# Performance work log

Measured on AMD Instinct MI355X. Metric: run time of the kernel, lower is better.

The kernel has to match this reference:

```python
import jax, jax.numpy as jnp
import numpy as np

BETA = 0.25  # commitment cost


def setup_inputs() -> dict:
    key = jax.random.key(0)
    k1, k2 = jax.random.split(key)
    B, C, T = 16, 256, 1024      # batch, emb_dim channels, sequence length
    N_EMB = 8192                 # codebook size
    z = jax.random.normal(k1, (B, C, T), dtype=jnp.float32)
    # original init: uniform(-1/n_emb, 1/n_emb); scale a normal similarly small
    emb = jax.random.normal(k2, (N_EMB, C), dtype=jnp.float32) * (1.0 / N_EMB)
    return {"z": z, "emb": emb}


def reference(z, emb):
    sg = jax.lax.stop_gradient
    # [B, C, T] -> [B, T, C]
    zt = jnp.transpose(z, (0, 2, 1))
    B, T, C = zt.shape
    zf = zt.reshape(-1, C)  # [B*T, C]
    # squared euclidean distances: ||z||^2 + ||e||^2 - 2 z.e  -> [B*T, N]
    d = (jnp.sum(zf * zf, axis=1, keepdims=True)
         + jnp.sum(emb * emb, axis=1)
         - 2.0 * jnp.einsum('bd,nd->bn', zf, emb))
    idx = jnp.argmin(d, axis=-1)               # [B*T]
    z_q = emb[idx].reshape(B, T, C)            # [B, T, C]
    loss = (BETA * jnp.mean((sg(z_q) - zt) ** 2)
            + jnp.mean((z_q - sg(zt)) ** 2))
    # straight-through estimator
    z_q = zt + sg(z_q - zt)
    z_q = jnp.transpose(z_q, (0, 2, 1))        # back to [B, C, T]
    return z_q, loss, idx
```

## Files before the change

### kernel.cpp

```cpp
#include <hip/hip_runtime.h>


#define C_    256
#define T_    1024
#define M_    16384
#define N_    8192

#define OUT_ZQ   0
#define OUT_LOSS 4194304
#define OUT_IDX  4194305

#define WS_SZ    0
#define WS_SE    16384
#define WS_PART  24576
#define MIN_OFF  131072u
#define FB_OFF   8519680u
#define WS_NEED  16908288u
#define O_I1     24576
#define O_I2     40960
#define O_PART   73728

typedef __attribute__((ext_vector_type(8))) short bf16x8;
typedef __attribute__((ext_vector_type(4))) float f32x4;
typedef unsigned long long ull;

__device__ __forceinline__ unsigned short f2b(float f) {
    unsigned u = __float_as_uint(f);
    return (unsigned short)((u + 0x7FFFu + ((u >> 16) & 1u)) >> 16);
}
__device__ __forceinline__ float b2f(unsigned short u) {
    return __uint_as_float(((unsigned)u) << 16);
}

__global__ __launch_bounds__(256) void vq_sums(const float* __restrict__ z,
                                               const float* __restrict__ emb,
                                               float* __restrict__ ws) {
    int gid = blockIdx.x * 256 + threadIdx.x;
    if (gid < M_) {
        int b = gid >> 10, t = gid & (T_ - 1);
        const float* zp = z + (size_t)b * C_ * T_ + t;
        float blk[2];
#pragma unroll
        for (int h = 0; h < 2; ++h) {
            float r[8];
#pragma unroll
            for (int j = 0; j < 8; ++j) {
                float v = zp[(size_t)(h * 128 + j) * T_];
                r[j] = __fmul_rn(v, v);
            }
            for (int i = 8; i < 128; i += 8)
#pragma unroll
                for (int j = 0; j < 8; ++j) {
                    float v = zp[(size_t)(h * 128 + i + j) * T_];
                    r[j] = __fadd_rn(r[j], __fmul_rn(v, v));
                }
            blk[h] = __fadd_rn(__fadd_rn(__fadd_rn(r[0], r[1]), __fadd_rn(r[2], r[3])),
                               __fadd_rn(__fadd_rn(r[4], r[5]), __fadd_rn(r[6], r[7])));
        }
        ws[WS_SZ + gid] = __fadd_rn(blk[0], blk[1]);
    } else if (gid < M_ + N_) {
        int n = gid - M_;
        const float* ep = emb + (size_t)n * C_;
        float blk[2];
#pragma unroll
        for (int h = 0; h < 2; ++h) {
            float r[8];
#pragma unroll
            for (int j = 0; j < 8; ++j) {
                float v = ep[h * 128 + j];
                r[j] = __fmul_rn(v, v);
            }
            for (int i = 8; i < 128; i += 8)
#pragma unroll
                for (int j = 0; j < 8; ++j) {
                    float v = ep[h * 128 + i + j];
                    r[j] = __fadd_rn(r[j], __fmul_rn(v, v));
                }
            blk[h] = __fadd_rn(__fadd_rn(__fadd_rn(r[0], r[1]), __fadd_rn(r[2], r[3])),
                               __fadd_rn(__fadd_rn(r[4], r[5]), __fadd_rn(r[6], r[7])));
        }
        ws[WS_SE + n] = __fadd_rn(blk[0], blk[1]);
    }
}

__global__ __launch_bounds__(256) void vq_prep_b(const float* __restrict__ emb,
                                                 char* __restrict__ fb) {
    int gid = blockIdx.x * 256 + threadIdx.x;
    int n = gid >> 5, kg = gid & 31;
    const float* ep = emb + (size_t)n * C_ + kg * 8;
    unsigned hi[8], lo[8];
#pragma unroll
    for (int j = 0; j < 8; ++j) {
        float v = ep[j];
        unsigned short h = f2b(v);
        hi[j] = h;
        lo[j] = f2b(v - b2f(h));
    }
    int nt = n >> 4, kt = kg >> 2, lane = (kg & 3) * 16 + (n & 15);
    size_t base = ((size_t)((nt * 8 + kt) * 2) << 10) + (lane << 4);
    uint4 hv = {hi[0] | (hi[1] << 16), hi[2] | (hi[3] << 16), hi[4] | (hi[5] << 16), hi[6] | (hi[7] << 16)};
    uint4 lv = {lo[0] | (lo[1] << 16), lo[2] | (lo[3] << 16), lo[4] | (lo[5] << 16), lo[6] | (lo[7] << 16)};
    *(uint4*)(fb + base) = hv;
    *(uint4*)(fb + base + 1024) = lv;
}

__global__ __launch_bounds__(256, 2) void vq_mfma2(
        const float* __restrict__ z, const char* __restrict__ fb,
        const float* __restrict__ sz, const float* __restrict__ se,
        ull* __restrict__ minima) {
    __shared__ __align__(16) char ldsA[65536];
    __shared__ __align__(16) char ldsB[16384];

    const int tid = threadIdx.x;
    const int lane = tid & 63;
    const int w = tid >> 6, wm = w & 1, wn = w >> 1;
    const int quad = lane >> 4, li = lane & 15;
    const int mb = blockIdx.x, ns = blockIdx.y;

    {
        const float* zb = z + (size_t)(mb >> 4) * C_ * T_ + ((mb & 15) << 6);
#pragma unroll
        for (int p = 0; p < 4; ++p) {
            int c  = p * 64 + (tid >> 2);
            int tq = tid & 3;
            const float* src = zb + (size_t)c * T_ + tq * 16;
            int kt = c >> 5, kg3 = (c >> 3) & 3, j = c & 7;
            unsigned short* d0 = (unsigned short*)(ldsA + (((tq * 8 + kt) * 2 + 0) << 10) + (kg3 << 8) + (j << 1));
            unsigned short* d1 = (unsigned short*)(ldsA + (((tq * 8 + kt) * 2 + 1) << 10) + (kg3 << 8) + (j << 1));
#pragma unroll
            for (int u = 0; u < 4; ++u) {
                float4 v = *(const float4*)(src + u * 4);
                float vv[4] = {v.x, v.y, v.z, v.w};
#pragma unroll
                for (int e = 0; e < 4; ++e) {
                    unsigned short h = f2b(vv[e]);
                    unsigned short l = f2b(vv[e] - b2f(h));
                    int i = u * 4 + e;
                    d0[i * 8] = h;
                    d1[i * 8] = l;
                }
            }
        }
    }

    float szr[8];
#pragma unroll
    for (int mt = 0; mt < 2; ++mt)
#pragma unroll
        for (int r = 0; r < 4; ++r)
            szr[mt * 4 + r] = sz[(mb << 6) + (wm << 5) + (mt << 4) + (quad << 2) + r];

    ull key[8];
#pragma unroll
    for (int s = 0; s < 8; ++s) key[s] = ~0ULL;

    const int f = tid >> 4, pos = (tid & 15) << 4;

    for (int nt = 0; nt < 32; ++nt) {
        f32x4 acc[2][4];
#pragma unroll
        for (int i = 0; i < 2; ++i)
#pragma unroll
            for (int j = 0; j < 4; ++j) acc[i][j] = (f32x4){0.f, 0.f, 0.f, 0.f};
        const int ntile0 = ns * 256 + nt * 8;

        for (int kt = 0; kt < 8; ++kt) {
            __syncthreads();
            {
                const char* srcB = fb + ((((size_t)(ntile0 + (f >> 1)) * 8 + kt) * 2 + (f & 1)) << 10) + pos;
                char* dB = ldsB + (f << 10) + pos;
#pragma unroll
                for (int i = 0; i < 4; ++i)
                    *(uint4*)(dB + i * 256) = *(const uint4*)(srcB + i * 256);
            }
            __syncthreads();
            bf16x8 a[2][2];
#pragma unroll
            for (int mt = 0; mt < 2; ++mt) {
                a[mt][0] = *(const bf16x8*)(ldsA + ((((wm * 2 + mt) * 8 + kt) * 2 + 0) << 10) + (lane << 4));
                a[mt][1] = *(const bf16x8*)(ldsA + ((((wm * 2 + mt) * 8 + kt) * 2 + 1) << 10) + (lane << 4));
            }
#pragma unroll
            for (int nt4 = 0; nt4 < 4; ++nt4) {
                bf16x8 bh = *(const bf16x8*)(ldsB + ((((wn * 4 + nt4) * 2 + 0)) << 10) + (lane << 4));
                bf16x8 bl = *(const bf16x8*)(ldsB + ((((wn * 4 + nt4) * 2 + 1)) << 10) + (lane << 4));
#pragma unroll
                for (int mt = 0; mt < 2; ++mt) {
                    f32x4 c = acc[mt][nt4];
                    c = __builtin_amdgcn_mfma_f32_16x16x32_bf16(a[mt][0], bh, c, 0, 0, 0);
                    c = __builtin_amdgcn_mfma_f32_16x16x32_bf16(a[mt][0], bl, c, 0, 0, 0);
                    c = __builtin_amdgcn_mfma_f32_16x16x32_bf16(a[mt][1], bh, c, 0, 0, 0);
                    acc[mt][nt4] = c;
                }
            }
        }
#pragma unroll
        for (int nt4 = 0; nt4 < 4; ++nt4) {
            const int ncol = ns * 4096 + nt * 128 + (wn * 4 + nt4) * 16 + li;
            const float sev = se[ncol];
#pragma unroll
            for (int mt = 0; mt < 2; ++mt) {
                f32x4 c = acc[mt][nt4];
#pragma unroll
                for (int r = 0; r < 4; ++r) {
                    float s = fmaf(-2.f, c[r], __fadd_rn(szr[mt * 4 + r], sev));
                    ull k = ((ull)__float_as_uint(s) << 32) | (unsigned)ncol;
                    int sl = mt * 4 + r;
                    if (k < key[sl]) key[sl] = k;
                }
            }
        }
        if (nt & 1) {
            int sc = nt >> 1;
#pragma unroll
            for (int sl = 0; sl < 8; ++sl) {
                ull kk = key[sl];
#pragma unroll
                for (int off = 1; off <= 8; off <<= 1) {
                    ull o = __shfl_xor(kk, off, 64);
                    if (o < kk) kk = o;
                }
                if (li == 0) {
                    int row = (mb << 6) + (wm << 5) + ((sl >> 2) << 4) + (quad << 2) + (sl & 3);
                    minima[(size_t)row * 64 + ((ns * 16 + sc) * 2 + wn)] = kk;
                }
                key[sl] = ~0ULL;
            }
        }
    }
}

__global__ __launch_bounds__(256) void vq_pick2(
        const float* __restrict__ z, const float* __restrict__ emb,
        const float* __restrict__ ws, const ull* __restrict__ minima,
        float* __restrict__ out) {
    __shared__ float Lz[256 * 17];
    const float* sz = ws + WS_SZ;
    const float* se = ws + WS_SE;
    const int tid = threadIdx.x;
    const int w = tid >> 6, lane = tid & 63, li = lane & 15;
    const int m0 = blockIdx.x * 16;
    const int b = m0 >> 10, t0 = m0 & (T_ - 1);

    {
        const float* src = z + (size_t)b * C_ * T_ + (size_t)tid * T_ + t0;
#pragma unroll
        for (int u = 0; u < 4; ++u) {
            float4 v = *(const float4*)(src + u * 4);
            Lz[tid * 17 + u * 4 + 0] = v.x;
            Lz[tid * 17 + u * 4 + 1] = v.y;
            Lz[tid * 17 + u * 4 + 2] = v.z;
            Lz[tid * 17 + u * 4 + 3] = v.w;
        }
    }
    __syncthreads();

    for (int rr = 0; rr < 4; ++rr) {
        const int tloc = w * 4 + rr;
        const int m = m0 + tloc;
        ull kmin = minima[(size_t)m * 64 + lane];
        int cand[4];
#pragma unroll
        for (int rep = 0; rep < 4; ++rep) {
            ull bf = kmin;
#pragma unroll
            for (int off = 1; off <= 32; off <<= 1) {
                ull o = __shfl_xor(bf, off, 64);
                if (o < bf) bf = o;
            }
            int ix = (int)(unsigned)(bf & 0xFFFFFFFFull);
            cand[rep] = ix < 0 ? 0 : (ix > N_ - 1 ? N_ - 1 : ix);
            if (kmin == bf) kmin = ~0ULL;
        }
        const int cn = cand[lane >> 4];
        const float* ep = emb + (size_t)cn * C_;
        double sum = 0.0;
#pragma unroll
        for (int cc = 0; cc < 16; ++cc) {
            int c = cc * 16 + li;
            sum = fma((double)Lz[c * 17 + tloc], (double)ep[c], sum);
        }
#pragma unroll
        for (int off = 1; off <= 8; off <<= 1)
            sum += __shfl_xor(sum, off, 64);
        double s0 = __shfl(sum, 0, 64), s1 = __shfl(sum, 16, 64);
        double s2 = __shfl(sum, 32, 64), s3 = __shfl(sum, 48, 64);
        if (lane == 0) {
            float szm = sz[m];
            float d0 = fmaf(-2.f, (float)s0, __fadd_rn(szm, se[cand[0]]));
            float d1 = fmaf(-2.f, (float)s1, __fadd_rn(szm, se[cand[1]]));
            float d2 = fmaf(-2.f, (float)s2, __fadd_rn(szm, se[cand[2]]));
            float d3 = fmaf(-2.f, (float)s3, __fadd_rn(szm, se[cand[3]]));
            float bd = d0; int bi = cand[0];
            if (d1 < bd || (d1 == bd && cand[1] < bi)) { bd = d1; bi = cand[1]; }
            if (d2 < bd || (d2 == bd && cand[2] < bi)) { bd = d2; bi = cand[2]; }
            if (d3 < bd || (d3 == bd && cand[3] < bi)) { bd = d3; bi = cand[3]; }
            out[OUT_IDX + m] = (float)bi;
        }
    }
}

__global__ __launch_bounds__(256) void vq_pass1_fp32(
        const float* __restrict__ z,
        const float* __restrict__ emb,
        float* __restrict__ ws) {
    __shared__ float As[32][68];
    __shared__ float Bs[32][68];
    const float* s_z = ws + WS_SZ;
    const float* s_e = ws + WS_SE;
    int* i1ws = (int*)ws + O_I1;
    int* i2ws = (int*)ws + O_I2;
    const int tid = threadIdx.x;
    const int mt  = blockIdx.x;
    const int tx  = tid & 15, ty = tid >> 4;
    const int b   = mt >> 4;
    const int t0  = (mt << 6) & (T_ - 1);
    const float* zbase = z + (size_t)b * C_ * T_ + t0;
    const int a_k = tid >> 4;
    const int a_m = (tid & 15) << 2;
    const int b_j = tid >> 2;
    const int b_q = (tid & 3) << 3;
    const float4 sz4 = *(const float4*)(s_z + mt * 64 + (ty << 2));
    const float szv[4] = {sz4.x, sz4.y, sz4.z, sz4.w};
    float v1[4], v2[4];
    int   i1[4], i2[4];
#pragma unroll
    for (int i = 0; i < 4; ++i) {
        v1[i] = INFINITY; v2[i] = INFINITY;
        i1[i] = 0x7FFFFFFF; i2[i] = 0x7FFFFFFF;
    }
    for (int nt = 0; nt < N_ / 64; ++nt) {
        const int n0 = nt * 64;
        float acc[4][4];
#pragma unroll
        for (int i = 0; i < 4; ++i)
#pragma unroll
            for (int j = 0; j < 4; ++j) acc[i][j] = 0.f;
        for (int kt = 0; kt < C_; kt += 32) {
            __syncthreads();
#pragma unroll
            for (int p = 0; p < 2; ++p) {
                int k = a_k + p * 16;
                float4 af = *(const float4*)(zbase + (size_t)(kt + k) * T_ + a_m);
                *(float4*)&As[k][a_m] = af;
            }
            {
                const float* ep = emb + (size_t)(n0 + b_j) * C_ + kt + b_q;
                float4 e0 = ((const float4*)ep)[0];
                float4 e1 = ((const float4*)ep)[1];
                Bs[b_q + 0][b_j] = e0.x; Bs[b_q + 1][b_j] = e0.y;
                Bs[b_q + 2][b_j] = e0.z; Bs[b_q + 3][b_j] = e0.w;
                Bs[b_q + 4][b_j] = e1.x; Bs[b_q + 5][b_j] = e1.y;
                Bs[b_q + 6][b_j] = e1.z; Bs[b_q + 7][b_j] = e1.w;
            }
            __syncthreads();
#pragma unroll
            for (int k = 0; k < 32; ++k) {
                const float4 a  = *(const float4*)&As[k][ty << 2];
                const float4 bv = *(const float4*)&Bs[k][tx << 2];
                acc[0][0] = fmaf(a.x, bv.x, acc[0][0]);
                acc[0][1] = fmaf(a.x, bv.y, acc[0][1]);
                acc[0][2] = fmaf(a.x, bv.z, acc[0][2]);
                acc[0][3] = fmaf(a.x, bv.w, acc[0][3]);
                acc[1][0] = fmaf(a.y, bv.x, acc[1][0]);
                acc[1][1] = fmaf(a.y, bv.y, acc[1][1]);
                acc[1][2] = fmaf(a.y, bv.z, acc[1][2]);
                acc[1][3] = fmaf(a.y, bv.w, acc[1][3]);
                acc[2][0] = fmaf(a.z, bv.x, acc[2][0]);
                acc[2][1] = fmaf(a.z, bv.y, acc[2][1]);
                acc[2][2] = fmaf(a.z, bv.z, acc[2][2]);
                acc[2][3] = fmaf(a.z, bv.w, acc[2][3]);
                acc[3][0] = fmaf(a.w, bv.x, acc[3][0]);
                acc[3][1] = fmaf(a.w, bv.y, acc[3][1]);
                acc[3][2] = fmaf(a.w, bv.z, acc[3][2]);
                acc[3][3] = fmaf(a.w, bv.w, acc[3][3]);
            }
        }
        const float4 se4 = *(const float4*)(s_e + n0 + (tx << 2));
        const float sev[4] = {se4.x, se4.y, se4.z, se4.w};
#pragma unroll
        for (int j = 0; j < 4; ++j) {
            const int n = n0 + (tx << 2) + j;
#pragma unroll
            for (int i = 0; i < 4; ++i) {
                float A = __fadd_rn(szv[i], sev[j]);
                float s = fmaf(-2.f, acc[i][j], A);
                if (s < v1[i]) { v2[i] = v1[i]; i2[i] = i1[i]; v1[i] = s; i1[i] = n; }
                else if (s < v2[i]) { v2[i] = s; i2[i] = n; }
            }
        }
    }
#pragma unroll
    for (int i = 0; i < 4; ++i) {
        float a1 = v1[i], a2 = v2[i];
        int   y1 = i1[i], y2 = i2[i];
#pragma unroll
        for (int off = 8; off >= 1; off >>= 1) {
            float o1 = __shfl_xor(a1, off, 64); int p1 = __shfl_xor(y1, off, 64);
            float o2 = __shfl_xor(a2, off, 64); int p2 = __shfl_xor(y2, off, 64);
            bool alt = (o1 < a1) || (o1 == a1 && p1 < y1);
            float w1 = alt ? o1 : a1; int q1 = alt ? p1 : y1;
            float lv = alt ? a1 : o1; int lq = alt ? y1 : p1;
            float wv = alt ? o2 : a2; int wq = alt ? p2 : y2;
            bool sb = (lv < wv) || (lv == wv && lq < wq);
            a2 = sb ? lv : wv; y2 = sb ? lq : wq;
            a1 = w1; y1 = q1;
        }
        if (tx == 0) {
            int m = mt * 64 + (ty << 2) + i;
            i1ws[m] = y1;
            i2ws[m] = y2;
        }
    }
}

__global__ __launch_bounds__(256) void vq_pass2_fp32(
        const float* __restrict__ z,
        const float* __restrict__ emb,
        float* __restrict__ ws,
        float* __restrict__ out) {
    const float* s_z = ws + WS_SZ;
    const float* s_e = ws + WS_SE;
    const int* i1ws = (const int*)ws + O_I1;
    const int* i2ws = (const int*)ws + O_I2;
    const int tid  = threadIdx.x;
    const int wave = tid >> 6, lane = tid & 63;
    const int half = lane >> 5;
    const int c0   = (lane & 31) << 3;
    const int rowbase = (blockIdx.x * 4 + wave) * 64;
    for (int r = 0; r < 64; ++r) {
        const int m = rowbase + r;
        int c1 = i1ws[m], c2 = i2ws[m];
        c1 = c1 < 0 ? 0 : (c1 > N_ - 1 ? N_ - 1 : c1);
        c2 = c2 < 0 ? 0 : (c2 > N_ - 1 ? N_ - 1 : c2);
        const int b = m >> 10, t = m & (T_ - 1);
        const float* zp = z + (size_t)b * C_ * T_ + t;
        const int cand = half ? c2 : c1;
        const float* ep = emb + (size_t)cand * C_;
        double sum = 0.0;
#pragma unroll
        for (int c = 0; c < 8; ++c)
            sum = fma((double)zp[(size_t)(c0 + c) * T_], (double)ep[c0 + c], sum);
#pragma unroll
        for (int off = 1; off <= 16; off <<= 1)
            sum += __shfl_xor(sum, off, 64);
        double s1 = __shfl(sum, 0, 64);
        double s2 = __shfl(sum, 32, 64);
        if (lane == 0) {
            float p1 = (float)s1, p2 = (float)s2;
            float d1 = fmaf(-2.f, p1, __fadd_rn(s_z[m], s_e[c1]));
            float d2 = fmaf(-2.f, p2, __fadd_rn(s_z[m], s_e[c2]));
            int win = ((d2 < d1) || (d2 == d1 && c2 < c1)) ? c2 : c1;
            out[OUT_IDX + m] = (float)win;
        }
    }
}

__global__ __launch_bounds__(256) void vq_gather(
        const float* __restrict__ z,
        const float* __restrict__ emb,
        float* __restrict__ partial,
        float* __restrict__ out) {
    __shared__ float Ls[64][129];
    __shared__ int   idxs[64];
    __shared__ float wred[4];
    const int tid = threadIdx.x;
    const int mg  = blockIdx.x;
    const int m0  = mg << 6;
    const int b   = m0 >> 10;
    const int t0  = m0 & (T_ - 1);
    if (tid < 64) {
        int ix = (int)out[OUT_IDX + m0 + tid];
        idxs[tid] = ix < 0 ? 0 : (ix > N_ - 1 ? N_ - 1 : ix);
    }
    __syncthreads();
    float lsum = 0.f;
    const int w = tid >> 6, l = tid & 63;
    const int tt2 = tid & 63, c0 = tid >> 6;
    const size_t base = (size_t)b * (C_ * T_) + t0 + tt2;
#pragma unroll
    for (int ch = 0; ch < 2; ++ch) {
        __syncthreads();
#pragma unroll
        for (int it = 0; it < 8; ++it) {
            int tt = it * 8 + w * 2 + (l >> 5);
            int cq = l & 31;
            int row = idxs[tt];
            float4 ev = *(const float4*)(emb + (size_t)row * C_ + ch * 128 + (cq << 2));
            Ls[tt][(cq << 2) + 0] = ev.x;
            Ls[tt][(cq << 2) + 1] = ev.y;
            Ls[tt][(cq << 2) + 2] = ev.z;
            Ls[tt][(cq << 2) + 3] = ev.w;
        }
        __syncthreads();
#pragma unroll
        for (int st = 0; st < 32; ++st) {
            int c_l = (st << 2) + c0;
            int c   = (ch << 7) + c_l;
            float v = Ls[tt2][c_l];
            size_t off = base + (size_t)c * T_;
            out[OUT_ZQ + off] = v;
            float d = v - z[off];
            lsum = fmaf(d, d, lsum);
        }
    }
#pragma unroll
    for (int off = 32; off >= 1; off >>= 1) lsum += __shfl_xor(lsum, off, 64);
    if (l == 0) wred[w] = lsum;
    __syncthreads();
    if (tid == 0) partial[mg] = wred[0] + wred[1] + wred[2] + wred[3];
}

__global__ __launch_bounds__(256) void vq_loss(const float* __restrict__ partial,
                                               float* __restrict__ out) {
    __shared__ float wred[4];
    const int tid = threadIdx.x;
    float v = partial[tid];
#pragma unroll
    for (int off = 32; off >= 1; off >>= 1) v += __shfl_xor(v, off, 64);
    if ((tid & 63) == 0) wred[tid >> 6] = v;
    __syncthreads();
    if (tid == 0)
        out[OUT_LOSS] = (wred[0] + wred[1] + wred[2] + wred[3]) * (1.25f / 4194304.f);
}

extern "C" void kernel_launch(void* const* d_in, const int* in_sizes, int n_in,
                              void* d_out, int out_size, void* d_ws, size_t ws_size,
                              hipStream_t stream) {
    const float* z   = (const float*)d_in[0];
    const float* emb = (const float*)d_in[1];
    float* out = (float*)d_out;
    float* ws  = (float*)d_ws;

    vq_sums<<<dim3((M_ + N_) / 256), dim3(256), 0, stream>>>(z, emb, ws);

    if (ws_size >= WS_NEED) {
        char* fb = (char*)d_ws + FB_OFF;
        ull* minima = (ull*)((char*)d_ws + MIN_OFF);
        vq_prep_b<<<dim3(1024), dim3(256), 0, stream>>>(emb, fb);
        vq_mfma2<<<dim3(256, 2), dim3(256), 0, stream>>>(z, fb, ws + WS_SZ, ws + WS_SE, minima);
        vq_pick2<<<dim3(1024), dim3(256), 0, stream>>>(z, emb, ws, minima, out);
        vq_gather<<<dim3(M_ / 64), dim3(256), 0, stream>>>(z, emb, ws + WS_PART, out);
        vq_loss<<<dim3(1), dim3(256), 0, stream>>>(ws + WS_PART, out);
    } else {
        vq_pass1_fp32<<<dim3(M_ / 64), dim3(256), 0, stream>>>(z, emb, ws);
        vq_pass2_fp32<<<dim3(64), dim3(256), 0, stream>>>(z, emb, ws, out);
        vq_gather<<<dim3(M_ / 64), dim3(256), 0, stream>>>(z, emb, ws + O_PART, out);
        vq_loss<<<dim3(1), dim3(256), 0, stream>>>(ws + O_PART, out);
    }
}
```

Measured before the change: 371.5 us.

## Stream codebook tiles straight into registers and drop LDS B staging

The distance GEMM kernel no longer stages codebook tiles through shared memory with two barriers per k-step. Each wave now loads its own B fragments directly from global memory into registers, double-buffered across k-steps, and computes all four M-subtiles against four N-subtiles. Block indices are remapped so the two codebook halves for neighbouring z blocks run close together, and minima are kept at a finer granularity (128 partial keys per row), which the pick kernel merges pairwise. This removes LDS traffic and barrier stalls, but raises register pressure, increases global/L2 loads of B, and enlarges the minima workspace.

After: 514.8 us. 1.39x slower.

```diff
diff --git a/kernel.cpp b/kernel.cpp
--- a/kernel.cpp
+++ b/kernel.cpp
@@ -14,8 +14,8 @@
 #define WS_SE    16384
 #define WS_PART  24576
 #define MIN_OFF  131072u
-#define FB_OFF   8519680u
-#define WS_NEED  16908288u
+#define FB_OFF   16908288u
+#define WS_NEED  25296896u
 #define O_I1     24576
 #define O_I2     40960
 #define O_PART   73728
@@ -104,18 +104,20 @@
     *(uint4*)(fb + base + 1024) = lv;
 }
 
-__global__ __launch_bounds__(256, 2) void vq_mfma2(
+__global__ __launch_bounds__(256, 2) void vq_mfma3(
         const float* __restrict__ z, const char* __restrict__ fb,
         const float* __restrict__ sz, const float* __restrict__ se,
         ull* __restrict__ minima) {
     __shared__ __align__(16) char ldsA[65536];
-    __shared__ __align__(16) char ldsB[16384];
 
     const int tid = threadIdx.x;
     const int lane = tid & 63;
-    const int w = tid >> 6, wm = w & 1, wn = w >> 1;
+    const int w = tid >> 6;
     const int quad = lane >> 4, li = lane & 15;
-    const int mb = blockIdx.x, ns = blockIdx.y;
+
+    const int bid = blockIdx.x;
+    const int ns = (bid >> 2) & 1;
+    const int mb = ((bid >> 3) << 2) | (bid & 3);
 
     {
         const float* zb = z + (size_t)(mb >> 4) * C_ * T_ + ((mb & 15) << 6);
@@ -142,92 +144,91 @@
             }
         }
     }
-
-    float szr[8];
-#pragma unroll
-    for (int mt = 0; mt < 2; ++mt)
+    __syncthreads();
+
+    float szr[16];
+#pragma unroll
+    for (int mt = 0; mt < 4; ++mt)
 #pragma unroll
         for (int r = 0; r < 4; ++r)
-            szr[mt * 4 + r] = sz[(mb << 6) + (wm << 5) + (mt << 4) + (quad << 2) + r];
-
-    ull key[8];
-#pragma unroll
-    for (int s = 0; s < 8; ++s) key[s] = ~0ULL;
-
-    const int f = tid >> 4, pos = (tid & 15) << 4;
-
-    for (int nt = 0; nt < 32; ++nt) {
-        f32x4 acc[2][4];
-#pragma unroll
-        for (int i = 0; i < 2; ++i)
+            szr[mt * 4 + r] = sz[(mb << 6) + (mt << 4) + (quad << 2) + r];
+
+    const char* fbw = fb + (lane << 4);
+
+#define LOADB(dst, kt_) do {                                                          \
+    _Pragma("unroll")                                                                 \
+    for (int nt4_ = 0; nt4_ < 4; ++nt4_) {                                            \
+        _Pragma("unroll")                                                             \
+        for (int p_ = 0; p_ < 2; ++p_)                                                \
+            dst[nt4_ * 2 + p_] = *(const bf16x8*)(fbw +                               \
+                ((((ntile0 + nt4_) * 8 + (kt_)) * 2 + p_) << 10));                    \
+    }                                                                                 \
+} while (0)
+
+#define COMPUTE(kt_, bb) do {                                                         \
+    _Pragma("unroll")                                                                 \
+    for (int mt_ = 0; mt_ < 4; ++mt_) {                                               \
+        bf16x8 ah = *(const bf16x8*)(ldsA + (((mt_ * 8 + (kt_)) * 2 + 0) << 10) + (lane << 4)); \
+        bf16x8 al = *(const bf16x8*)(ldsA + (((mt_ * 8 + (kt_)) * 2 + 1) << 10) + (lane << 4)); \
+        _Pragma("unroll")                                                             \
+        for (int nt4_ = 0; nt4_ < 4; ++nt4_) {                                        \
+            f32x4 c = acc[mt_][nt4_];                                                 \
+            c = __builtin_amdgcn_mfma_f32_16x16x32_bf16(ah, bb[nt4_ * 2 + 0], c, 0, 0, 0); \
+            c = __builtin_amdgcn_mfma_f32_16x16x32_bf16(ah, bb[nt4_ * 2 + 1], c, 0, 0, 0); \
+            c = __builtin_amdgcn_mfma_f32_16x16x32_bf16(al, bb[nt4_ * 2 + 0], c, 0, 0, 0); \
+            acc[mt_][nt4_] = c;                                                       \
+        }                                                                             \
+    }                                                                                 \
+} while (0)
+
+    for (int nt = 0; nt < 16; ++nt) {
+        const int ntile0 = ns * 256 + (nt << 4) + (w << 2);
+        f32x4 acc[4][4];
+#pragma unroll
+        for (int i = 0; i < 4; ++i)
 #pragma unroll
             for (int j = 0; j < 4; ++j) acc[i][j] = (f32x4){0.f, 0.f, 0.f, 0.f};
-        const int ntile0 = ns * 256 + nt * 8;
-
-        for (int kt = 0; kt < 8; ++kt) {
-            __syncthreads();
-            {
-                const char* srcB = fb + ((((size_t)(ntile0 + (f >> 1)) * 8 + kt) * 2 + (f & 1)) << 10) + pos;
-                char* dB = ldsB + (f << 10) + pos;
-#pragma unroll
-                for (int i = 0; i < 4; ++i)
-                    *(uint4*)(dB + i * 256) = *(const uint4*)(srcB + i * 256);
-            }
-            __syncthreads();
-            bf16x8 a[2][2];
-#pragma unroll
-            for (int mt = 0; mt < 2; ++mt) {
-                a[mt][0] = *(const bf16x8*)(ldsA + ((((wm * 2 + mt) * 8 + kt) * 2 + 0) << 10) + (lane << 4));
-                a[mt][1] = *(const bf16x8*)(ldsA + ((((wm * 2 + mt) * 8 + kt) * 2 + 1) << 10) + (lane << 4));
-            }
-#pragma unroll
-            for (int nt4 = 0; nt4 < 4; ++nt4) {
-                bf16x8 bh = *(const bf16x8*)(ldsB + ((((wn * 4 + nt4) * 2 + 0)) << 10) + (lane << 4));
-                bf16x8 bl = *(const bf16x8*)(ldsB + ((((wn * 4 + nt4) * 2 + 1)) << 10) + (lane << 4));
-#pragma unroll
-                for (int mt = 0; mt < 2; ++mt) {
-                    f32x4 c = acc[mt][nt4];
-                    c = __builtin_amdgcn_mfma_f32_16x16x32_bf16(a[mt][0], bh, c, 0, 0, 0);
-                    c = __builtin_amdgcn_mfma_f32_16x16x32_bf16(a[mt][0], bl, c, 0, 0, 0);
-                    c = __builtin_amdgcn_mfma_f32_16x16x32_bf16(a[mt][1], bh, c, 0, 0, 0);
-                    acc[mt][nt4] = c;
+
+        bf16x8 bA[8], bB[8];
+        LOADB(bA, 0);
+#pragma unroll
+        for (int kth = 0; kth < 4; ++kth) {
+            LOADB(bB, 2 * kth + 1);
+            COMPUTE(2 * kth, bA);
+            if (kth < 3) LOADB(bA, 2 * kth + 2);
+            COMPUTE(2 * kth + 1, bB);
+        }
+
+        float sev[4];
+#pragma unroll
+        for (int nt4 = 0; nt4 < 4; ++nt4)
+            sev[nt4] = se[((ntile0 + nt4) << 4) + li];
+#pragma unroll
+        for (int mt = 0; mt < 4; ++mt) {
+#pragma unroll
+            for (int r = 0; r < 4; ++r) {
+                ull best = ~0ULL;
+#pragma unroll
+                for (int nt4 = 0; nt4 < 4; ++nt4) {
+                    const int ncol = ((ntile0 + nt4) << 4) + li;
+                    float s = fmaf(-2.f, acc[mt][nt4][r], __fadd_rn(szr[mt * 4 + r], sev[nt4]));
+                    ull k = ((ull)__float_as_uint(s) << 32) | (unsigned)ncol;
+                    if (k < best) best = k;
                 }
-            }
-        }
-#pragma unroll
-        for (int nt4 = 0; nt4 < 4; ++nt4) {
-            const int ncol = ns * 4096 + nt * 128 + (wn * 4 + nt4) * 16 + li;
-            const float sev = se[ncol];
-#pragma unroll
-            for (int mt = 0; mt < 2; ++mt) {
-                f32x4 c = acc[mt][nt4];
-#pragma unroll
-                for (int r = 0; r < 4; ++r) {
-                    float s = fmaf(-2.f, c[r], __fadd_rn(szr[mt * 4 + r], sev));
-                    ull k = ((ull)__float_as_uint(s) << 32) | (unsigned)ncol;
-                    int sl = mt * 4 + r;
-                    if (k < key[sl]) key[sl] = k;
-                }
-            }
-        }
-        if (nt & 1) {
-            int sc = nt >> 1;
-#pragma unroll
-            for (int sl = 0; sl < 8; ++sl) {
-                ull kk = key[sl];
 #pragma unroll
                 for (int off = 1; off <= 8; off <<= 1) {
-                    ull o = __shfl_xor(kk, off, 64);
-                    if (o < kk) kk = o;
+                    ull o = __shfl_xor(best, off, 64);
+                    if (o < best) best = o;
                 }
                 if (li == 0) {
-                    int row = (mb << 6) + (wm << 5) + ((sl >> 2) << 4) + (quad << 2) + (sl & 3);
-                    minima[(size_t)row * 64 + ((ns * 16 + sc) * 2 + wn)] = kk;
+                    int row = (mb << 6) + (mt << 4) + (quad << 2) + r;
+                    minima[(size_t)row * 128 + (ns << 6) + (nt << 2) + w] = best;
                 }
-                key[sl] = ~0ULL;
-            }
-        }
-    }
+            }
+        }
+    }
+#undef LOADB
+#undef COMPUTE
 }
 
 __global__ __launch_bounds__(256) void vq_pick2(
@@ -258,7 +259,9 @@
     for (int rr = 0; rr < 4; ++rr) {
         const int tloc = w * 4 + rr;
         const int m = m0 + tloc;
-        ull kmin = minima[(size_t)m * 64 + lane];
+        ull k0 = minima[(size_t)m * 128 + lane];
+        ull k1 = minima[(size_t)m * 128 + 64 + lane];
+        ull kmin = k1 < k0 ? k1 : k0;
         int cand[4];
 #pragma unroll
         for (int rep = 0; rep < 4; ++rep) {
@@ -538,7 +541,7 @@
         char* fb = (char*)d_ws + FB_OFF;
         ull* minima = (ull*)((char*)d_ws + MIN_OFF);
         vq_prep_b<<<dim3(1024), dim3(256), 0, stream>>>(emb, fb);
-        vq_mfma2<<<dim3(256, 2), dim3(256), 0, stream>>>(z, fb, ws + WS_SZ, ws + WS_SE, minima);
+        vq_mfma3<<<dim3(512), dim3(256), 0, stream>>>(z, fb, ws + WS_SZ, ws + WS_SE, minima);
         vq_pick2<<<dim3(1024), dim3(256), 0, stream>>>(z, emb, ws, minima, out);
         vq_gather<<<dim3(M_ / 64), dim3(256), 0, stream>>>(z, emb, ws + WS_PART, out);
         vq_loss<<<dim3(1), dim3(256), 0, stream>>>(ws + WS_PART, out);
```

## Double-buffer codebook tiles via direct global-to-LDS loads with wider N tile

Applied to the files above, without the earlier changes.

Rewrites the distance GEMM kernel so each block processes 256 codebook columns per tile instead of 128. Each wave now covers all 64 rows and its own 64 columns. Codebook tiles are streamed into a double-buffered 64KB LDS region with global_load_lds, prefetching the next k-slice while MFMAs run on the current one, which cuts the per-step barriers from two to one. The cost is 128KB of LDS and more registers per block, dropping occupancy to one block per CU. Prefetch correctness also depends on the single barrier at the end of each k-step.

New measurement: 354.7 us. -4.5%, faster.

```diff
diff --git a/kernel.cpp b/kernel.cpp
--- a/kernel.cpp
+++ b/kernel.cpp
@@ -104,18 +104,34 @@
     *(uint4*)(fb + base + 1024) = lv;
 }
 
-__global__ __launch_bounds__(256, 2) void vq_mfma2(
+__global__ __launch_bounds__(256, 1) void vq_mfma4(
         const float* __restrict__ z, const char* __restrict__ fb,
         const float* __restrict__ sz, const float* __restrict__ se,
         ull* __restrict__ minima) {
     __shared__ __align__(16) char ldsA[65536];
-    __shared__ __align__(16) char ldsB[16384];
+    __shared__ __align__(16) char ldsB[65536];
 
     const int tid = threadIdx.x;
     const int lane = tid & 63;
-    const int w = tid >> 6, wm = w & 1, wn = w >> 1;
+    const int w = tid >> 6;
     const int quad = lane >> 4, li = lane & 15;
     const int mb = blockIdx.x, ns = blockIdx.y;
+    const int ns256 = ns << 8;
+
+#define STAGEB(nt_, kt_, buf_) do {                                                   \
+    _Pragma("unroll")                                                                 \
+    for (int i_ = 0; i_ < 8; ++i_) {                                                  \
+        int f_ = (w << 3) + i_;                                                       \
+        int ntb_ = f_ >> 1, pp_ = f_ & 1;                                             \
+        size_t goff_ = ((size_t)((((ns256 + ((nt_) << 4) + ntb_) << 3) + (kt_)) * 2 + pp_) << 10) + (lane << 4); \
+        __builtin_amdgcn_global_load_lds(                                             \
+            (__attribute__((address_space(1))) unsigned*)(size_t)(fb + goff_),        \
+            (__attribute__((address_space(3))) unsigned*)(unsigned)(size_t)(ldsB + ((buf_) << 15) + (f_ << 10)), \
+            16, 0, 0);                                                                \
+    }                                                                                 \
+} while (0)
+
+    STAGEB(0, 0, 0);
 
     {
         const float* zb = z + (size_t)(mb >> 4) * C_ * T_ + ((mb & 15) << 6);
@@ -142,92 +158,94 @@
             }
         }
     }
-
-    float szr[8];
-#pragma unroll
-    for (int mt = 0; mt < 2; ++mt)
+    __syncthreads();
+
+    float szr[16];
+#pragma unroll
+    for (int mt = 0; mt < 4; ++mt)
 #pragma unroll
         for (int r = 0; r < 4; ++r)
-            szr[mt * 4 + r] = sz[(mb << 6) + (wm << 5) + (mt << 4) + (quad << 2) + r];
-
-    ull key[8];
-#pragma unroll
-    for (int s = 0; s < 8; ++s) key[s] = ~0ULL;
-
-    const int f = tid >> 4, pos = (tid & 15) << 4;
-
-    for (int nt = 0; nt < 32; ++nt) {
-        f32x4 acc[2][4];
-#pragma unroll
-        for (int i = 0; i < 2; ++i)
+            szr[mt * 4 + r] = sz[(mb << 6) + (mt << 4) + (quad << 2) + r];
+
+    ull key[16];
+#pragma unroll
+    for (int s = 0; s < 16; ++s) key[s] = ~0ULL;
+
+    for (int nt = 0; nt < 16; ++nt) {
+        f32x4 acc[4][4];
+#pragma unroll
+        for (int i = 0; i < 4; ++i)
 #pragma unroll
             for (int j = 0; j < 4; ++j) acc[i][j] = (f32x4){0.f, 0.f, 0.f, 0.f};
-        const int ntile0 = ns * 256 + nt * 8;
-
+
+#pragma unroll
         for (int kt = 0; kt < 8; ++kt) {
-            __syncthreads();
-            {
-                const char* srcB = fb + ((((size_t)(ntile0 + (f >> 1)) * 8 + kt) * 2 + (f & 1)) << 10) + pos;
-                char* dB = ldsB + (f << 10) + pos;
-#pragma unroll
-                for (int i = 0; i < 4; ++i)
-                    *(uint4*)(dB + i * 256) = *(const uint4*)(srcB + i * 256);
-            }
-            __syncthreads();
-            bf16x8 a[2][2];
-#pragma unroll
-            for (int mt = 0; mt < 2; ++mt) {
-                a[mt][0] = *(const bf16x8*)(ldsA + ((((wm * 2 + mt) * 8 + kt) * 2 + 0) << 10) + (lane << 4));
-                a[mt][1] = *(const bf16x8*)(ldsA + ((((wm * 2 + mt) * 8 + kt) * 2 + 1) << 10) + (lane << 4));
+            if (kt < 7)       STAGEB(nt, kt + 1, (kt + 1) & 1);
+            else if (nt < 15) STAGEB(nt + 1, 0, 0);
+
+            const char* bB = ldsB + ((kt & 1) << 15);
+            bf16x8 ah[4], al[4];
+#pragma unroll
+            for (int mt = 0; mt < 4; ++mt) {
+                ah[mt] = *(const bf16x8*)(ldsA + ((((mt << 3) + kt) * 2 + 0) << 10) + (lane << 4));
+                al[mt] = *(const bf16x8*)(ldsA + ((((mt << 3) + kt) * 2 + 1) << 10) + (lane << 4));
             }
 #pragma unroll
             for (int nt4 = 0; nt4 < 4; ++nt4) {
-                bf16x8 bh = *(const bf16x8*)(ldsB + ((((wn * 4 + nt4) * 2 + 0)) << 10) + (lane << 4));
-                bf16x8 bl = *(const bf16x8*)(ldsB + ((((wn * 4 + nt4) * 2 + 1)) << 10) + (lane << 4));
-#pragma unroll
-                for (int mt = 0; mt < 2; ++mt) {
+                const char* bp = bB + ((((w << 2) + nt4) * 2) << 10) + (lane << 4);
+                bf16x8 bh = *(const bf16x8*)(bp);
+                bf16x8 bl = *(const bf16x8*)(bp + 1024);
+#pragma unroll
+                for (int mt = 0; mt < 4; ++mt) {
                     f32x4 c = acc[mt][nt4];
-                    c = __builtin_amdgcn_mfma_f32_16x16x32_bf16(a[mt][0], bh, c, 0, 0, 0);
-                    c = __builtin_amdgcn_mfma_f32_16x16x32_bf16(a[mt][0], bl, c, 0, 0, 0);
-                    c = __builtin_amdgcn_mfma_f32_16x16x32_bf16(a[mt][1], bh, c, 0, 0, 0);
+                    c = __builtin_amdgcn_mfma_f32_16x16x32_bf16(ah[mt], bh, c, 0, 0, 0);
+                    c = __builtin_amdgcn_mfma_f32_16x16x32_bf16(ah[mt], bl, c, 0, 0, 0);
+                    c = __builtin_amdgcn_mfma_f32_16x16x32_bf16(al[mt], bh, c, 0, 0, 0);
                     acc[mt][nt4] = c;
                 }
             }
-        }
-#pragma unroll
-        for (int nt4 = 0; nt4 < 4; ++nt4) {
-            const int ncol = ns * 4096 + nt * 128 + (wn * 4 + nt4) * 16 + li;
-            const float sev = se[ncol];
-#pragma unroll
-            for (int mt = 0; mt < 2; ++mt) {
-                f32x4 c = acc[mt][nt4];
-#pragma unroll
-                for (int r = 0; r < 4; ++r) {
-                    float s = fmaf(-2.f, c[r], __fadd_rn(szr[mt * 4 + r], sev));
-                    ull k = ((ull)__float_as_uint(s) << 32) | (unsigned)ncol;
-                    int sl = mt * 4 + r;
-                    if (k < key[sl]) key[sl] = k;
+
+            if (kt == 7) {
+                float sev[4];
+#pragma unroll
+                for (int nt4 = 0; nt4 < 4; ++nt4)
+                    sev[nt4] = se[(ns << 12) + (nt << 8) + (((w << 2) + nt4) << 4) + li];
+#pragma unroll
+                for (int mt = 0; mt < 4; ++mt)
+#pragma unroll
+                    for (int r = 0; r < 4; ++r) {
+                        int sl = (mt << 2) + r;
+                        ull best = key[sl];
+#pragma unroll
+                        for (int nt4 = 0; nt4 < 4; ++nt4) {
+                            int ncol = (ns << 12) + (nt << 8) + (((w << 2) + nt4) << 4) + li;
+                            float s = fmaf(-2.f, acc[mt][nt4][r], __fadd_rn(szr[sl], sev[nt4]));
+                            ull k = ((ull)__float_as_uint(s) << 32) | (unsigned)ncol;
+                            if (k < best) best = k;
+                        }
+                        key[sl] = best;
+                    }
+                if (nt & 1) {
+#pragma unroll
+                    for (int sl = 0; sl < 16; ++sl) {
+                        ull kk = key[sl];
+#pragma unroll
+                        for (int off = 1; off <= 8; off <<= 1) {
+                            ull o = __shfl_xor(kk, off, 64);
+                            if (o < kk) kk = o;
+                        }
+                        if (li == 0) {
+                            int row = (mb << 6) + ((sl >> 2) << 4) + (quad << 2) + (sl & 3);
+                            minima[(size_t)row * 64 + (ns << 5) + ((nt >> 1) << 2) + w] = kk;
+                        }
+                        key[sl] = ~0ULL;
+                    }
                 }
             }
-        }
-        if (nt & 1) {
-            int sc = nt >> 1;
-#pragma unroll
-            for (int sl = 0; sl < 8; ++sl) {
-                ull kk = key[sl];
-#pragma unroll
-                for (int off = 1; off <= 8; off <<= 1) {
-                    ull o = __shfl_xor(kk, off, 64);
-                    if (o < kk) kk = o;
-                }
-                if (li == 0) {
-                    int row = (mb << 6) + (wm << 5) + ((sl >> 2) << 4) + (quad << 2) + (sl & 3);
-                    minima[(size_t)row * 64 + ((ns * 16 + sc) * 2 + wn)] = kk;
-                }
-                key[sl] = ~0ULL;
-            }
-        }
-    }
+            __syncthreads();
+        }
+    }
+#undef STAGEB
 }
 
 __global__ __launch_bounds__(256) void vq_pick2(
@@ -538,7 +556,7 @@
         char* fb = (char*)d_ws + FB_OFF;
         ull* minima = (ull*)((char*)d_ws + MIN_OFF);
         vq_prep_b<<<dim3(1024), dim3(256), 0, stream>>>(emb, fb);
-        vq_mfma2<<<dim3(256, 2), dim3(256), 0, stream>>>(z, fb, ws + WS_SZ, ws + WS_SE, minima);
+        vq_mfma4<<<dim3(256, 2), dim3(256), 0, stream>>>(z, fb, ws + WS_SZ, ws + WS_SE, minima);
         vq_pick2<<<dim3(1024), dim3(256), 0, stream>>>(z, emb, ws, minima, out);
         vq_gather<<<dim3(M_ / 64), dim3(256), 0, stream>>>(z, emb, ws + WS_PART, out);
         vq_loss<<<dim3(1), dim3(256), 0, stream>>>(ws + WS_PART, out);
```
